# Performance work log

Measured on AMD Instinct MI355X. Metric: run time of the kernel, lower is better.

Reference implementation:

```python
import jax, jax.numpy as jnp
import numpy as np

B, N, E = 128, 2000, 2000
EMBED, HIDDEN = 256, 512


def setup_inputs() -> dict:
    key = jax.random.key(0)
    k1, k2, k3, k4, k5, k6, k7 = jax.random.split(key, 7)
    node_embeddings = jax.random.normal(k1, (B, N, EMBED), dtype=jnp.float32)
    locs = jax.random.uniform(k2, (B, N, 2), dtype=jnp.float32)
    edge_list = jax.random.randint(k3, (B, E, 2), 0, N, dtype=jnp.int64)
    in_dim = 2 * EMBED + 1
    # Kaiming-ish init for the two Linear layers of edge_scorer
    W1 = jax.random.normal(k4, (in_dim, HIDDEN), dtype=jnp.float32) / np.sqrt(in_dim)
    b1 = jnp.zeros((HIDDEN,), dtype=jnp.float32)
    W2 = jax.random.normal(k5, (HIDDEN, 1), dtype=jnp.float32) / np.sqrt(HIDDEN)
    b2 = jnp.zeros((1,), dtype=jnp.float32)
    return {
        "node_embeddings": node_embeddings,
        "locs": locs,
        "edge_list": edge_list,
        "delete_bias": 0,
        "W1": W1,
        "b1": b1,
        "W2": W2,
        "b2": b2,
    }


def reference(node_embeddings, locs, edge_list, delete_bias, W1, b1, W2, b2):
    # valid mask for -1-padded edges
    valid = (edge_list[..., 0] >= 0) & (edge_list[..., 1] >= 0)  # (B, E)
    edges = jnp.clip(edge_list, 0, None)
    bidx = jnp.arange(node_embeddings.shape[0])[:, None]  # (B, 1)
    i, j = edges[..., 0], edges[..., 1]  # (B, E)
    emb_i = node_embeddings[bidx, i]  # (B, E, D)
    emb_j = node_embeddings[bidx, j]  # (B, E, D)
    d = locs[bidx, i] - locs[bidx, j]  # (B, E, 2)
    dist = jnp.sqrt(jnp.sum(d * d, axis=-1, keepdims=True))  # (B, E, 1)
    feats = jnp.concatenate([emb_i, emb_j, dist], axis=-1)  # (B, E, 2D+1)
    h = jax.nn.relu(jnp.einsum('bef,fh->beh', feats, W1) + b1)
    logits = (jnp.einsum('beh,ho->beo', h, W2) + b2)[..., 0]  # (B, E)
    logits = jnp.where(valid, logits, -jnp.inf)
    return logits + jnp.float32(delete_bias)
```

## Files before the change

kernel.cpp:

```cpp
#include <hip/hip_runtime.h>
#include <math.h>

#define EMBED    256
#define HIDDEN   512
#define KDIM     512
#define Nn       2000
#define Ee       2000
#define BM       128
#define NTHREADS 512
#define NBLK     2000
#define PITCH    72

typedef __attribute__((ext_vector_type(8)))  short bf16x8;
typedef __attribute__((ext_vector_type(16))) float f32x16;

static __device__ __forceinline__ short f2bf(float f) {
  unsigned u = __builtin_bit_cast(unsigned, f);
  u += 0x7fffu + ((u >> 16) & 1u);
  return (short)(u >> 16);
}

static __device__ __forceinline__ bf16x8 cvt8(float4 a, float4 b) {
  bf16x8 v;
  v[0]=f2bf(a.x); v[1]=f2bf(a.y); v[2]=f2bf(a.z); v[3]=f2bf(a.w);
  v[4]=f2bf(b.x); v[5]=f2bf(b.y); v[6]=f2bf(b.z); v[7]=f2bf(b.w);
  return v;
}

__global__ void w1f_kernel(const float* __restrict__ W1, short* __restrict__ W1F) {
  const int t  = blockIdx.x * 512 + threadIdx.x;
  const int l  = t & 63;
  const int tk = (t >> 6) & 31;
  const int tn = t >> 11;
  const int n  = tn * 32 + (l & 31);
  const int k0 = tk * 16 + (l >> 5) * 8;
  bf16x8 v;
#pragma unroll
  for (int q = 0; q < 8; ++q)
    v[q] = f2bf(W1[(size_t)(k0 + q) * HIDDEN + n]);
  *(bf16x8*)(W1F + (size_t)t * 8) = v;
}

__global__ __launch_bounds__(NTHREADS, 2)
void edge_kernel(const float* __restrict__ emb, const float* __restrict__ locs,
                 const int* __restrict__ edges, const int* __restrict__ dbias,
                 const float* __restrict__ W1, const float* __restrict__ b1,
                 const float* __restrict__ W2, const float* __restrict__ b2,
                 const short* __restrict__ W1F, float* __restrict__ out)
{
  __shared__ short  feat[2][BM][PITCH];
  __shared__ float4 ep_s[HIDDEN];
  __shared__ float  part_s[8][BM];
  __shared__ float  dist_s[BM];
  __shared__ int    valid_s[BM];
  __shared__ int    ibase_s[BM];
  __shared__ int    jbase_s[BM];

  const int tid = threadIdx.x;

  const int wg = (blockIdx.x & 7) * (NBLK / 8) + (blockIdx.x >> 3);

  if (tid < BM) {
    const int g  = wg * BM + tid;
    const int b  = g / Ee;
    const int i0 = edges[2 * g];
    const int j0 = edges[2 * g + 1];
    valid_s[tid] = (i0 >= 0) && (j0 >= 0);
    const int ib = b * Nn + (i0 < 0 ? 0 : i0);
    const int jb = b * Nn + (j0 < 0 ? 0 : j0);
    ibase_s[tid] = ib;
    jbase_s[tid] = jb;
    const float dx = locs[2 * (size_t)ib]     - locs[2 * (size_t)jb];
    const float dy = locs[2 * (size_t)ib + 1] - locs[2 * (size_t)jb + 1];
    dist_s[tid] = sqrtf(dx * dx + dy * dy);
  }
  ep_s[tid] = make_float4(b1[tid], W1[(size_t)KDIM * HIDDEN + tid], W2[tid], 0.f);
  asm volatile("s_waitcnt lgkmcnt(0)" ::: "memory");
  __builtin_amdgcn_s_barrier();
  asm volatile("" ::: "memory");

  const int e  = tid >> 2;
  const int sq = tid & 3;

  const int lane = tid & 63;
  const int ng   = tid >> 6;
  const int ln31 = lane & 31;
  const int kg   = lane >> 5;

  {
    const float* p = emb + (size_t)ibase_s[e] * EMBED + sq * 16;
    float4 v0 = *(const float4*)(p);
    float4 v1 = *(const float4*)(p + 4);
    float4 v2 = *(const float4*)(p + 8);
    float4 v3 = *(const float4*)(p + 12);
    *(bf16x8*)&feat[0][e][sq * 16]     = cvt8(v0, v1);
    *(bf16x8*)&feat[0][e][sq * 16 + 8] = cvt8(v2, v3);
  }
  bf16x8 wc0[4], wc1[4];
  {
    const short* wb = W1F + (size_t)(ng * 64) * 512 + lane * 8;
#pragma unroll
    for (int ks = 0; ks < 4; ++ks) {
      wc0[ks] = *(const bf16x8*)(wb + ks * 512);
      wc1[ks] = *(const bf16x8*)(wb + 32 * 512 + ks * 512);
    }
  }
  float4 g0, g1, g2, g3;
  {
    const float* p = emb + (size_t)ibase_s[e] * EMBED + 64 + sq * 16;
    g0 = *(const float4*)(p);
    g1 = *(const float4*)(p + 4);
    g2 = *(const float4*)(p + 8);
    g3 = *(const float4*)(p + 12);
  }
  asm volatile("s_waitcnt lgkmcnt(0)" ::: "memory");
  __builtin_amdgcn_s_barrier();
  asm volatile("" ::: "memory");

  f32x16 acc[4][2];
#pragma unroll
  for (int et = 0; et < 4; ++et)
#pragma unroll
    for (int nt = 0; nt < 2; ++nt)
#pragma unroll
      for (int q = 0; q < 16; ++q) acc[et][nt][q] = 0.f;

#pragma unroll 1
  for (int c = 0; c < 8; ++c) {
    const int bb = c & 1;
    const int nbuf = bb ^ 1;

    bf16x8 wn0[4], wn1[4];
    if (c < 7) {
      const short* wb = W1F + (size_t)(ng * 64 + (c + 1) * 4) * 512 + lane * 8;
#pragma unroll
      for (int ks = 0; ks < 4; ++ks) {
        wn0[ks] = *(const bf16x8*)(wb + ks * 512);
        wn1[ks] = *(const bf16x8*)(wb + 32 * 512 + ks * 512);
      }
    }

#pragma unroll
    for (int ks = 0; ks < 4; ++ks) {
#pragma unroll
      for (int et = 0; et < 4; ++et) {
        bf16x8 fb = *(const bf16x8*)(&feat[bb][et * 32 + ln31][ks * 16 + kg * 8]);
        acc[et][0] = __builtin_amdgcn_mfma_f32_32x32x16_bf16(wc0[ks], fb, acc[et][0], 0, 0, 0);
        acc[et][1] = __builtin_amdgcn_mfma_f32_32x32x16_bf16(wc1[ks], fb, acc[et][1], 0, 0, 0);
      }
    }

    if (c < 7) {
      *(bf16x8*)&feat[nbuf][e][sq * 16]     = cvt8(g0, g1);
      *(bf16x8*)&feat[nbuf][e][sq * 16 + 8] = cvt8(g2, g3);
    }

    __builtin_amdgcn_sched_barrier(0);
    if (c < 6) {
      const int cc = c + 2;
      const int rb = (cc < 4) ? ibase_s[e] : jbase_s[e];
      const float* p = emb + (size_t)rb * EMBED + (cc & 3) * 64 + sq * 16;
      g0 = *(const float4*)(p);
      g1 = *(const float4*)(p + 4);
      g2 = *(const float4*)(p + 8);
      g3 = *(const float4*)(p + 12);
    }
    __builtin_amdgcn_sched_barrier(0);

    asm volatile("s_waitcnt lgkmcnt(0)" ::: "memory");
    __builtin_amdgcn_s_barrier();
    asm volatile("" ::: "memory");

#pragma unroll
    for (int ks = 0; ks < 4; ++ks) { wc0[ks] = wn0[ks]; wc1[ks] = wn1[ks]; }
  }

  float dv[4], ps[4];
#pragma unroll
  for (int et = 0; et < 4; ++et) {
    dv[et] = dist_s[et * 32 + ln31];
    ps[et] = 0.f;
  }
#pragma unroll
  for (int nt = 0; nt < 2; ++nt) {
#pragma unroll
    for (int r = 0; r < 16; ++r) {
      const int n = ng * 64 + nt * 32 + (r & 3) + ((r >> 2) << 3) + (kg << 2);
      const float4 ep = ep_s[n];
#pragma unroll
      for (int et = 0; et < 4; ++et) {
        float p = acc[et][nt][r] + ep.x + dv[et] * ep.y;
        ps[et] += fmaxf(p, 0.f) * ep.z;
      }
    }
  }
#pragma unroll
  for (int et = 0; et < 4; ++et) ps[et] += __shfl_xor(ps[et], 32, 64);
  if (lane < 32) {
#pragma unroll
    for (int et = 0; et < 4; ++et) part_s[ng][et * 32 + ln31] = ps[et];
  }
  __syncthreads();

  if (tid < BM) {
    float s = 0.f;
#pragma unroll
    for (int w = 0; w < 8; ++w) s += part_s[w][tid];
    float logit = s + b2[0] + (float)dbias[0];
    if (!valid_s[tid]) logit = -__builtin_inff();
    out[(size_t)wg * BM + tid] = logit;
  }
}

extern "C" void kernel_launch(void* const* d_in, const int* in_sizes, int n_in,
                              void* d_out, int out_size, void* d_ws, size_t ws_size,
                              hipStream_t stream) {
  const float* emb   = (const float*)d_in[0];
  const float* locs  = (const float*)d_in[1];
  const int*   edges = (const int*)d_in[2];
  const int*   dbias = (const int*)d_in[3];
  const float* W1    = (const float*)d_in[4];
  const float* b1    = (const float*)d_in[5];
  const float* W2    = (const float*)d_in[6];
  const float* b2    = (const float*)d_in[7];
  float*       out   = (float*)d_out;
  short*       W1F   = (short*)d_ws;

  w1f_kernel<<<dim3(64), dim3(512), 0, stream>>>(W1, W1F);
  edge_kernel<<<dim3(NBLK), dim3(NTHREADS), 0, stream>>>(
      emb, locs, edges, dbias, W1, b1, W2, b2, (const short*)W1F, out);
}
```

Measured before the change: 163.4 us.

## Stage half the K dimension at once in MFMA-fragment LDS layout

Result: slower. 198.0 us (+21.2%).

```diff
diff --git a/kernel.cpp b/kernel.cpp
--- a/kernel.cpp
+++ b/kernel.cpp
@@ -3,13 +3,12 @@
 
 #define EMBED    256
 #define HIDDEN   512
-#define KDIM     512
 #define Nn       2000
 #define Ee       2000
 #define BM       128
 #define NTHREADS 512
 #define NBLK     2000
-#define PITCH    72
+#define KSTEPS   16
 
 typedef __attribute__((ext_vector_type(8)))  short bf16x8;
 typedef __attribute__((ext_vector_type(16))) float f32x16;
@@ -48,13 +47,11 @@
                  const float* __restrict__ W2, const float* __restrict__ b2,
                  const short* __restrict__ W1F, float* __restrict__ out)
 {
-  __shared__ short  feat[2][BM][PITCH];
-  __shared__ float4 ep_s[HIDDEN];
-  __shared__ float  part_s[8][BM];
-  __shared__ float  dist_s[BM];
-  __shared__ int    valid_s[BM];
-  __shared__ int    ibase_s[BM];
-  __shared__ int    jbase_s[BM];
+  __shared__ short ffrag[KSTEPS * 4 * 64 * 8];
+  __shared__ float b1_s[HIDDEN], w513_s[HIDDEN], w2_s[HIDDEN];
+  __shared__ float part_s[8][BM];
+  __shared__ float dist_s[BM];
+  __shared__ int   valid_s[BM], ibase_s[BM], jbase_s[BM];
 
   const int tid = threadIdx.x;
 
@@ -74,48 +71,21 @@
     const float dy = locs[2 * (size_t)ib + 1] - locs[2 * (size_t)jb + 1];
     dist_s[tid] = sqrtf(dx * dx + dy * dy);
   }
-  ep_s[tid] = make_float4(b1[tid], W1[(size_t)KDIM * HIDDEN + tid], W2[tid], 0.f);
-  asm volatile("s_waitcnt lgkmcnt(0)" ::: "memory");
-  __builtin_amdgcn_s_barrier();
-  asm volatile("" ::: "memory");
+  b1_s[tid]   = b1[tid];
+  w513_s[tid] = W1[(size_t)512 * HIDDEN + tid];
+  w2_s[tid]   = W2[tid];
+  __syncthreads();
 
   const int e  = tid >> 2;
   const int sq = tid & 3;
 
   const int lane = tid & 63;
-  const int ng   = tid >> 6;
+  const int w    = tid >> 6;
   const int ln31 = lane & 31;
   const int kg   = lane >> 5;
 
-  {
-    const float* p = emb + (size_t)ibase_s[e] * EMBED + sq * 16;
-    float4 v0 = *(const float4*)(p);
-    float4 v1 = *(const float4*)(p + 4);
-    float4 v2 = *(const float4*)(p + 8);
-    float4 v3 = *(const float4*)(p + 12);
-    *(bf16x8*)&feat[0][e][sq * 16]     = cvt8(v0, v1);
-    *(bf16x8*)&feat[0][e][sq * 16 + 8] = cvt8(v2, v3);
-  }
-  bf16x8 wc0[4], wc1[4];
-  {
-    const short* wb = W1F + (size_t)(ng * 64) * 512 + lane * 8;
-#pragma unroll
-    for (int ks = 0; ks < 4; ++ks) {
-      wc0[ks] = *(const bf16x8*)(wb + ks * 512);
-      wc1[ks] = *(const bf16x8*)(wb + 32 * 512 + ks * 512);
-    }
-  }
-  float4 g0, g1, g2, g3;
-  {
-    const float* p = emb + (size_t)ibase_s[e] * EMBED + 64 + sq * 16;
-    g0 = *(const float4*)(p);
-    g1 = *(const float4*)(p + 4);
-    g2 = *(const float4*)(p + 8);
-    g3 = *(const float4*)(p + 12);
-  }
-  asm volatile("s_waitcnt lgkmcnt(0)" ::: "memory");
-  __builtin_amdgcn_s_barrier();
-  asm volatile("" ::: "memory");
+  const float* rowi = emb + (size_t)ibase_s[e] * EMBED + sq * 64;
+  const float* rowj = emb + (size_t)jbase_s[e] * EMBED + sq * 64;
 
   f32x16 acc[4][2];
 #pragma unroll
@@ -126,53 +96,46 @@
       for (int q = 0; q < 16; ++q) acc[et][nt][q] = 0.f;
 
 #pragma unroll 1
-  for (int c = 0; c < 8; ++c) {
-    const int bb = c & 1;
-    const int nbuf = bb ^ 1;
-
-    bf16x8 wn0[4], wn1[4];
-    if (c < 7) {
-      const short* wb = W1F + (size_t)(ng * 64 + (c + 1) * 4) * 512 + lane * 8;
+  for (int ph = 0; ph < 2; ++ph) {
+    {
+      const float* src = ph == 0 ? rowi : rowj;
+      const int et = e >> 5;
+      const int es = e & 31;
 #pragma unroll
-      for (int ks = 0; ks < 4; ++ks) {
-        wn0[ks] = *(const bf16x8*)(wb + ks * 512);
-        wn1[ks] = *(const bf16x8*)(wb + 32 * 512 + ks * 512);
+      for (int gph = 0; gph < 2; ++gph) {
+        float4 t[8];
+#pragma unroll
+        for (int q = 0; q < 8; ++q) t[q] = *(const float4*)(src + gph * 32 + 4 * q);
+#pragma unroll
+        for (int p = 0; p < 4; ++p) {
+          const int j  = gph * 4 + p;
+          const int ks = sq * 4 + (j >> 1);
+          const int dst16 = ((ks * 4 + et) * 64 + (j & 1) * 32 + es);
+          *(bf16x8*)&ffrag[dst16 * 8] = cvt8(t[2 * p], t[2 * p + 1]);
+        }
       }
     }
+    __syncthreads();
 
+    const short* wb = W1F + ((size_t)(w * 2) * 32 + ph * 16) * 512 + lane * 8;
+    bf16x8 wc0 = *(const bf16x8*)(wb);
+    bf16x8 wc1 = *(const bf16x8*)(wb + 32 * 512);
 #pragma unroll
-    for (int ks = 0; ks < 4; ++ks) {
+    for (int ks = 0; ks < KSTEPS; ++ks) {
+      bf16x8 wn0, wn1;
+      if (ks < KSTEPS - 1) {
+        wn0 = *(const bf16x8*)(wb + (ks + 1) * 512);
+        wn1 = *(const bf16x8*)(wb + 32 * 512 + (ks + 1) * 512);
+      }
 #pragma unroll
       for (int et = 0; et < 4; ++et) {
-        bf16x8 fb = *(const bf16x8*)(&feat[bb][et * 32 + ln31][ks * 16 + kg * 8]);
-        acc[et][0] = __builtin_amdgcn_mfma_f32_32x32x16_bf16(wc0[ks], fb, acc[et][0], 0, 0, 0);
-        acc[et][1] = __builtin_amdgcn_mfma_f32_32x32x16_bf16(wc1[ks], fb, acc[et][1], 0, 0, 0);
+        bf16x8 fb = *(const bf16x8*)(&ffrag[((ks * 4 + et) * 64 + lane) * 8]);
+        acc[et][0] = __builtin_amdgcn_mfma_f32_32x32x16_bf16(wc0, fb, acc[et][0], 0, 0, 0);
+        acc[et][1] = __builtin_amdgcn_mfma_f32_32x32x16_bf16(wc1, fb, acc[et][1], 0, 0, 0);
       }
+      wc0 = wn0; wc1 = wn1;
     }
-
-    if (c < 7) {
-      *(bf16x8*)&feat[nbuf][e][sq * 16]     = cvt8(g0, g1);
-      *(bf16x8*)&feat[nbuf][e][sq * 16 + 8] = cvt8(g2, g3);
-    }
-
-    __builtin_amdgcn_sched_barrier(0);
-    if (c < 6) {
-      const int cc = c + 2;
-      const int rb = (cc < 4) ? ibase_s[e] : jbase_s[e];
-      const float* p = emb + (size_t)rb * EMBED + (cc & 3) * 64 + sq * 16;
-      g0 = *(const float4*)(p);
-      g1 = *(const float4*)(p + 4);
-      g2 = *(const float4*)(p + 8);
-      g3 = *(const float4*)(p + 12);
-    }
-    __builtin_amdgcn_sched_barrier(0);
-
-    asm volatile("s_waitcnt lgkmcnt(0)" ::: "memory");
-    __builtin_amdgcn_s_barrier();
-    asm volatile("" ::: "memory");
-
-#pragma unroll
-    for (int ks = 0; ks < 4; ++ks) { wc0[ks] = wn0[ks]; wc1[ks] = wn1[ks]; }
+    __syncthreads();
   }
 
   float dv[4], ps[4];
@@ -185,12 +148,14 @@
   for (int nt = 0; nt < 2; ++nt) {
 #pragma unroll
     for (int r = 0; r < 16; ++r) {
-      const int n = ng * 64 + nt * 32 + (r & 3) + ((r >> 2) << 3) + (kg << 2);
-      const float4 ep = ep_s[n];
+      const int n = w * 64 + nt * 32 + (r & 3) + ((r >> 2) << 3) + (kg << 2);
+      const float bias = b1_s[n];
+      const float wd   = w513_s[n];
+      const float w2v  = w2_s[n];
 #pragma unroll
       for (int et = 0; et < 4; ++et) {
-        float p = acc[et][nt][r] + ep.x + dv[et] * ep.y;
-        ps[et] += fmaxf(p, 0.f) * ep.z;
+        float p = acc[et][nt][r] + bias + dv[et] * wd;
+        ps[et] += fmaxf(p, 0.f) * w2v;
       }
     }
   }
@@ -198,14 +163,14 @@
   for (int et = 0; et < 4; ++et) ps[et] += __shfl_xor(ps[et], 32, 64);
   if (lane < 32) {
 #pragma unroll
-    for (int et = 0; et < 4; ++et) part_s[ng][et * 32 + ln31] = ps[et];
+    for (int et = 0; et < 4; ++et) part_s[w][et * 32 + ln31] = ps[et];
   }
   __syncthreads();
 
   if (tid < BM) {
     float s = 0.f;
 #pragma unroll
-    for (int w = 0; w < 8; ++w) s += part_s[w][tid];
+    for (int wv = 0; wv < 8; ++wv) s += part_s[wv][tid];
     float logit = s + b2[0] + (float)dbias[0];
     if (!valid_s[tid]) logit = -__builtin_inff();
     out[(size_t)wg * BM + tid] = logit;
```
